# Kernel optimization log

Measured on AMD Instinct MI355X. Metric: run time of the kernel, lower is better.

The kernel has to match this reference:

```python
import jax, jax.numpy as jnp
import numpy as np
import math

D = 1024
H = 16
DH = D // H
B = 4
NSEQ = 1024
NSEG = 2
EXP = 4


def layer_norm(x, w, b=None, eps=1e-5):
    mu = jnp.mean(x, axis=-1, keepdims=True)
    var = jnp.mean((x - mu) ** 2, axis=-1, keepdims=True)
    y = (x - mu) * jax.lax.rsqrt(var + eps) * w
    return y + b if b is not None else y


def apply_rope(x, positions):
    # x: [B, L, H, Dh]; ESM-style rotate-half RoPE
    dh = x.shape[-1]
    inv_freq = 1.0 / (10000.0 ** (jnp.arange(0, dh, 2, dtype=jnp.float32) / dh))
    freqs = positions.astype(jnp.float32)[:, None] * inv_freq[None, :]  # [L, Dh/2]
    emb = jnp.concatenate([freqs, freqs], axis=-1)  # [L, Dh]
    cos = jnp.cos(emb)[None, :, None, :]
    sin = jnp.sin(emb)[None, :, None, :]
    x1, x2 = jnp.split(x, 2, axis=-1)
    return x * cos + jnp.concatenate([-x2, x1], axis=-1) * sin


def timestep_embedding(timesteps, embedding_dim=256, max_len=10000):
    # timesteps: [N]
    ts = timesteps * max_len
    half = embedding_dim // 2
    emb = math.log(max_len) / (half - 1)
    freqs = jnp.exp(jnp.arange(half, dtype=jnp.float32) * -emb)
    e = ts.astype(jnp.float32)[:, None] * freqs[None, :]
    return jnp.concatenate([jnp.sin(e), jnp.cos(e)], axis=1)  # [N, 256]


def make_autoregressive_attn_mask(batch_mask, n_seg):
    b, n_res = batch_mask.shape
    L = (n_seg + 1) * n_res
    causal = jnp.tril(jnp.ones((L, L), dtype=bool))[None, None]  # [1,1,L,L]
    tiled = jnp.tile(batch_mask, (1, n_seg + 1)).astype(bool)  # [B, L]
    key_valid = tiled[:, None, None, :]
    q_valid = tiled[:, None, :, None]
    allowed = causal & key_valid & q_valid  # [B,1,L,L]
    first_edit = (batch_mask[:, None, :] * batch_mask[:, :, None]).astype(bool)
    allowed = allowed.at[:, 0, :n_res, :n_res].set(first_edit)
    return allowed


def setup_inputs() -> dict:
    key = jax.random.key(0)
    ks = jax.random.split(key, 32)
    s = 0.02
    p = lambda i, shape: jax.random.normal(ks[i], shape, dtype=jnp.float32) * s
    inp = {
        'x_seq': jax.random.normal(ks[0], (B, NSEQ, D), dtype=jnp.float32),
        'x_struc': jax.random.normal(ks[1], (B, 1, D), dtype=jnp.float32),
        'temp': jax.random.uniform(ks[2], (B, 1, 1), dtype=jnp.float32),
        'mask': jnp.ones((B, NSEQ), dtype=jnp.float32),
        'ln_qs_w': jnp.ones((D,), jnp.float32), 'ln_qs_b': jnp.zeros((D,), jnp.float32),
        'W_qkv_seq': p(3, (D, 3 * D)),
        'ln_qt_w': jnp.ones((D,), jnp.float32), 'ln_qt_b': jnp.zeros((D,), jnp.float32),
        'W_qkv_struc': p(4, (D, 3 * D)),
        'q_ln_seq_w': jnp.ones((D,), jnp.float32), 'k_ln_seq_w': jnp.ones((D,), jnp.float32),
        'q_ln_struc_w': jnp.ones((D,), jnp.float32), 'k_ln_struc_w': jnp.ones((D,), jnp.float32),
        'W_out_seq': p(5, (D, D)), 'W_out_struc': p(6, (D, D)),
        'temp_w1': p(7, (1, D)), 'temp_b1': jnp.zeros((D,), jnp.float32),
        'temp_w2': p(8, (D, D)), 'temp_b2': jnp.zeros((D,), jnp.float32),
        'T_w1': p(9, (256, D)), 'T_b1': jnp.zeros((D,), jnp.float32),
        'T_w2': p(10, (D, D)), 'T_b2': jnp.zeros((D,), jnp.float32),
        'ffn_seq_ln_w': jnp.ones((D,), jnp.float32), 'ffn_seq_ln_b': jnp.zeros((D,), jnp.float32),
        'ffn_seq_w1': p(11, (D, EXP * D)), 'ffn_seq_w2': p(12, (EXP * D, D)),
        'ffn_struc_ln_w': jnp.ones((D,), jnp.float32), 'ffn_struc_ln_b': jnp.zeros((D,), jnp.float32),
        'ffn_struc_w1': p(13, (D, EXP * D)), 'ffn_struc_w2': p(14, (EXP * D, D)),
        'T': 1,
    }
    return inp


def reference(x_seq, x_struc, temp, mask,
              ln_qs_w, ln_qs_b, W_qkv_seq,
              ln_qt_w, ln_qt_b, W_qkv_struc,
              q_ln_seq_w, k_ln_seq_w, q_ln_struc_w, k_ln_struc_w,
              W_out_seq, W_out_struc,
              temp_w1, temp_b1, temp_w2, temp_b2,
              T_w1, T_b1, T_w2, T_b2,
              ffn_seq_ln_w, ffn_seq_ln_b, ffn_seq_w1, ffn_seq_w2,
              ffn_struc_ln_w, ffn_struc_ln_b, ffn_struc_w1, ffn_struc_w2,
              T):
    b, n_seq, d = x_seq.shape
    n_seg, index = NSEG, 0  # index=0 prefill path

    # --- seq track QKV (index == 0 only) ---
    qkv_seq = layer_norm(x_seq, ln_qs_w, ln_qs_b) @ W_qkv_seq
    q_s, k_s, v_s = jnp.split(qkv_seq, 3, axis=-1)
    q_s = layer_norm(q_s, q_ln_seq_w)
    k_s = layer_norm(k_s, k_ln_seq_w)
    pos_seq = jnp.arange(n_seq)
    q_s = apply_rope(q_s.reshape(b, n_seq, H, DH), pos_seq).reshape(b, n_seq, d)
    k_s = apply_rope(k_s.reshape(b, n_seq, H, DH), pos_seq).reshape(b, n_seq, d)

    # --- struc track conditioning + QKV ---
    position_T = jnp.arange(n_seg, dtype=jnp.float32) * T / 100.0
    T_input = jnp.repeat(position_T, n_seq)[index:index + 1]  # [1]
    x_norm = layer_norm(x_struc, ln_qt_w, ln_qt_b)
    temp_e = jax.nn.silu(temp @ temp_w1 + temp_b1) @ temp_w2 + temp_b2  # [B,1,D]
    t_emb = timestep_embedding(T_input)  # [1,256]
    T_e = jax.nn.silu(t_emb @ T_w1 + T_b1) @ T_w2 + T_b2  # [1,D]
    x_mod = x_norm + temp_e + T_e[None, :, :]
    qkv_t = x_mod @ W_qkv_struc
    q_t, k_t, v_t = jnp.split(qkv_t, 3, axis=-1)
    q_t = layer_norm(q_t, q_ln_struc_w)
    k_t = layer_norm(k_t, k_ln_struc_w)
    pos_res = jnp.tile(jnp.arange(n_seq), n_seg)[index:index + 1]  # [1]
    q_t = apply_rope(q_t.reshape(b, 1, H, DH), pos_res).reshape(b, 1, d)
    k_t = apply_rope(k_t.reshape(b, 1, H, DH), pos_res).reshape(b, 1, d)

    # --- KV cache contents for index 0: [seq tokens, struc token] ---
    keys = jnp.concatenate([k_s, k_t], axis=1)    # [B, N_seq+1, D]
    values = jnp.concatenate([v_s, v_t], axis=1)
    queries = jnp.concatenate([q_s, q_t], axis=1)

    to_heads = lambda t: t.reshape(b, -1, H, DH).transpose(0, 2, 1, 3)  # b h s d
    qh, kh, vh = to_heads(queries), to_heads(keys), to_heads(values)

    allowed = make_autoregressive_attn_mask(mask, n_seg)  # [B,1,L,L]
    Lq = n_seq + index + 1
    attn_mask = allowed[:, :, :Lq, :Lq]

    scale = 1.0 / math.sqrt(DH)
    scores = jnp.einsum('bhqd,bhkd->bhqk', qh, kh) * scale
    scores = jnp.where(attn_mask, scores, -1e9)
    probs = jax.nn.softmax(scores, axis=-1)
    ctx = jnp.einsum('bhqk,bhkd->bhqd', probs, vh)
    ctx = ctx.transpose(0, 2, 1, 3).reshape(b, Lq, d)

    out_seq = ctx[:, :n_seq] @ W_out_seq
    out_struc = ctx[:, n_seq:] @ W_out_struc

    # residuals (scaling_factor = 1)
    x_seq = x_seq + out_seq
    x_struc = x_struc + out_struc

    # GELU FFNs (LN -> Linear -> GELU -> Linear, no bias)
    h_seq = jax.nn.gelu(layer_norm(x_seq, ffn_seq_ln_w, ffn_seq_ln_b) @ ffn_seq_w1, approximate=False) @ ffn_seq_w2
    x_seq = x_seq + h_seq
    h_struc = jax.nn.gelu(layer_norm(x_struc, ffn_struc_ln_w, ffn_struc_ln_b) @ ffn_struc_w1, approximate=False) @ ffn_struc_w2
    x_struc = x_struc + h_struc

    return (x_seq, x_struc)
```

## Files before the change

kernel.cpp:

```cpp
#include <hip/hip_runtime.h>

typedef __attribute__((ext_vector_type(8))) short short8;
typedef __attribute__((ext_vector_type(4))) float f32x4;
typedef __attribute__((ext_vector_type(4))) unsigned short us4;

#define DEV static __device__ __forceinline__

DEV float bf2f(unsigned short u){ union{unsigned u; float f;} v; v.u=((unsigned)u)<<16; return v.f; }
DEV unsigned short f2bf(float f){ union{float f; unsigned u;} v; v.f=f; unsigned r=v.u+0x7fffu+((v.u>>16)&1u); return (unsigned short)(r>>16); }
DEV unsigned short f2bf_t(float f){ union{float f; unsigned u;} v; v.f=f; return (unsigned short)(v.u>>16); }
DEV float gelu_f(float x){ return 0.5f*x*(1.0f+erff(x*0.7071067811865475f)); }
DEV float silu_f(float x){ return x/(1.0f+__expf(-x)); }

DEV void gload16(const void* g, void* l){
  __builtin_amdgcn_global_load_lds((const __attribute__((address_space(1))) void*)g,
                                   (__attribute__((address_space(3))) void*)l, 16, 0, 0);
}

DEV void blk_reduce2(float &a, float &b){
  #pragma unroll
  for (int off=32; off>0; off>>=1){ a += __shfl_down(a,off); b += __shfl_down(b,off); }
  __shared__ float sa[4], sb[4];
  int w=threadIdx.x>>6;
  if((threadIdx.x&63)==0){ sa[w]=a; sb[w]=b; }
  __syncthreads();
  a=sa[0]+sa[1]+sa[2]+sa[3]; b=sb[0]+sb[1]+sb[2]+sb[3];
}

template<int OUTF32>
__global__ __launch_bounds__(256) void ln_rows(const float* __restrict__ x,
    const float* __restrict__ w, const float* __restrict__ bias, void* __restrict__ outp)
{
  int row=blockIdx.x, t=threadIdx.x;
  const float* xr = x + (size_t)row*1024;
  float4 v = *(const float4*)(xr + t*4);
  float s=v.x+v.y+v.z+v.w;
  float s2=v.x*v.x+v.y*v.y+v.z*v.z+v.w*v.w;
  blk_reduce2(s,s2);
  float mu=s*(1.0f/1024.0f);
  float rs=rsqrtf(s2*(1.0f/1024.0f)-mu*mu+1e-5f);
  int d0=t*4;
  const float* vp=(const float*)&v;
  float y[4];
  #pragma unroll
  for(int j=0;j<4;j++){ float bb = bias? bias[d0+j] : 0.0f; y[j]=(vp[j]-mu)*rs*w[d0+j]+bb; }
  if (OUTF32){
    float4 o; o.x=y[0];o.y=y[1];o.z=y[2];o.w=y[3];
    *(float4*)((float*)outp + (size_t)row*1024 + d0) = o;
  } else {
    us4 o;
    #pragma unroll
    for(int j=0;j<4;j++) o[j]=f2bf(y[j]);
    *(us4*)((unsigned short*)outp + (size_t)row*1024 + d0) = o;
  }
}

__global__ __launch_bounds__(256) void wtrans(const float* __restrict__ Bm,
    unsigned short* __restrict__ Bt, int K, int N)
{
  __shared__ float tile[32][33];
  int nb = blockIdx.x*32, kb = blockIdx.y*32;
  int tx = threadIdx.x&31, ty = threadIdx.x>>5;
  #pragma unroll
  for(int i=0;i<32;i+=8) tile[ty+i][tx] = Bm[(size_t)(kb+ty+i)*N + nb+tx];
  __syncthreads();
  #pragma unroll
  for(int i=0;i<32;i+=8) Bt[(size_t)(nb+ty+i)*K + kb+tx] = f2bf(tile[tx][ty+i]);
}

__global__ __launch_bounds__(256) void vtrans(const unsigned short* __restrict__ qkv,
    unsigned short* __restrict__ vT)
{
  __shared__ unsigned short tile[32][33];
  int d0 = blockIdx.x*32, tk0 = blockIdx.y*32, b = blockIdx.z;
  int tx = threadIdx.x&31, ty = threadIdx.x>>5;
  #pragma unroll
  for(int i=0;i<32;i+=8) tile[ty+i][tx] = qkv[(size_t)(b*1024+tk0+ty+i)*3072 + 2048 + d0+tx];
  __syncthreads();
  #pragma unroll
  for(int i=0;i<32;i+=8) vT[(size_t)(b*1024+d0+ty+i)*1024 + tk0+tx] = tile[tx][ty+i];
}

__global__ void rope_table(float* __restrict__ tab){
  int idx = blockIdx.x*256 + threadIdx.x;
  if (idx >= 1024*32) return;
  int pos = idx>>5, i = idx&31;
  float inv = exp2f(-(float)i * (13.287712379549449f/32.0f));
  float a = (float)pos*inv;
  tab[idx*2]   = cosf(a);
  tab[idx*2+1] = sinf(a);
}

__global__ __launch_bounds__(256) void qk_ln_rope(
    const unsigned short* __restrict__ qkv, const float* __restrict__ qw, const float* __restrict__ kw,
    const float* __restrict__ tab, unsigned short* __restrict__ qr, unsigned short* __restrict__ kr)
{
  __shared__ float lnr[1024];
  int row=blockIdx.x, part=blockIdx.y, t=threadIdx.x;
  const unsigned short* src = qkv + (size_t)row*3072 + part*1024 + t*4;
  us4 u = *(const us4*)src;
  float x[4];
  #pragma unroll
  for(int j=0;j<4;j++) x[j]=bf2f(u[j]);
  float s=x[0]+x[1]+x[2]+x[3];
  float s2=x[0]*x[0]+x[1]*x[1]+x[2]*x[2]+x[3]*x[3];
  blk_reduce2(s,s2);
  float mu=s*(1.0f/1024.0f);
  float rsg=rsqrtf(s2*(1.0f/1024.0f)-mu*mu+1e-5f);
  const float* w = part? kw : qw;
  int d0=t*4;
  #pragma unroll
  for(int j=0;j<4;j++) lnr[d0+j]=(x[j]-mu)*rsg*w[d0+j];
  __syncthreads();
  int n = row & 1023;
  unsigned short* dst = (part? kr: qr) + (size_t)row*1024 + d0;
  us4 o;
  #pragma unroll
  for(int j=0;j<4;j++){
    int d=d0+j, dh=d&63, fi=dh&31;
    float c=tab[(n*32+fi)*2], sn=tab[(n*32+fi)*2+1];
    float p=lnr[d^32];
    o[j]=f2bf(lnr[d]*c + ((dh<32)? -p : p)*sn);
  }
  *(us4*)dst = o;
}

template<int EPI>
__global__ __launch_bounds__(512) void gemm256(
    const unsigned short* __restrict__ A, int lda,
    const unsigned short* __restrict__ Bt, int ldb,
    int N, int K, void* Cout)
{
  __shared__ unsigned short As[16384];
  __shared__ unsigned short Bs[16384];
  const int t=threadIdx.x;
  int GX=gridDim.x, GY=gridDim.y, nwg=GX*GY;
  int bx, by;
  if (!(nwg&7)){
    int d = blockIdx.y*GX + blockIdx.x;
    int g = (d&7)*(nwg>>3) + (d>>3);
    bx = g%GX; by = g/GX;
  } else { bx = blockIdx.x; by = blockIdx.y; }
  const int m0=by*256, n0=bx*256;
  const int l=t&63, w=t>>6, lg=l>>4, lr=l&15;
  const int wr=w>>2, wc=w&3;
  const int srow=t>>3, sseg=(t&7)^((t>>3)&7);
  const f32x4 z4 = {0.f,0.f,0.f,0.f};
  f32x4 acc[8][4];
  #pragma unroll
  for(int i=0;i<8;i++)
    #pragma unroll
    for(int j=0;j<4;j++) acc[i][j]=z4;
  for (int k0=0;k0<K;k0+=64){
    __syncthreads();
    #pragma unroll
    for(int i=0;i<4;i++){
      gload16(A  + (size_t)(m0+srow+i*64)*lda + k0 + sseg*8, As + i*4096 + w*512);
      gload16(Bt + (size_t)(n0+srow+i*64)*ldb + k0 + sseg*8, Bs + i*4096 + w*512);
    }
    __syncthreads();
    #pragma unroll
    for(int ks=0;ks<2;ks++){
      short8 a[8], bfr[4];
      #pragma unroll
      for(int m=0;m<8;m++){
        int row=wr*128+m*16+lr;
        a[m] = *(const short8*)&As[row*64 + ((ks*4+lg)^(row&7))*8];
      }
      #pragma unroll
      for(int n=0;n<4;n++){
        int row=wc*64+n*16+lr;
        bfr[n] = *(const short8*)&Bs[row*64 + ((ks*4+lg)^(row&7))*8];
      }
      #pragma unroll
      for(int m=0;m<8;m++)
        #pragma unroll
        for(int n=0;n<4;n++)
          acc[m][n] = __builtin_amdgcn_mfma_f32_16x16x32_bf16(a[m], bfr[n], acc[m][n], 0,0,0);
    }
  }
  #pragma unroll
  for(int m=0;m<8;m++){
    #pragma unroll
    for(int n=0;n<4;n++){
      #pragma unroll
      for(int r=0;r<4;r++){
        int row=m0+wr*128+m*16+lg*4+r, col=n0+wc*64+n*16+lr;
        size_t idx=(size_t)row*N+col;
        float v=acc[m][n][r];
        if (EPI==2){ ((unsigned short*)Cout)[idx] = f2bf(gelu_f(v)); }
        else { ((unsigned short*)Cout)[idx] = f2bf(v); }
      }
    }
  }
}

template<int EPI>
__global__ __launch_bounds__(256) void gemm_bt(
    const unsigned short* __restrict__ A, int lda,
    const unsigned short* __restrict__ Bt, int ldb,
    int N, int K, void* Cout, const float* resp, void* Cout2)
{
  __shared__ unsigned short As[8192];
  __shared__ unsigned short Bs[8192];
  const int t=threadIdx.x;
  int GX=gridDim.x, GY=gridDim.y, nwg=GX*GY;
  int m0, n0;
  if (!((GX&7) || (nwg&63))){
    int d = blockIdx.y*GX + blockIdx.x;
    int xcd = d&7, j = d>>3;
    int g = xcd*(nwg>>3) + j;
    int chunk = g>>6, local = g&63;
    int chunks_x = GX>>3;
    int cx = chunk%chunks_x, cy = chunk/chunks_x;
    n0 = (cx*8 + (local&7))*128;
    m0 = (cy*8 + (local>>3))*128;
  } else {
    m0 = blockIdx.y*128; n0 = blockIdx.x*128;
  }
  const int kofs = blockIdx.z*K;
  unsigned short* Cb = (unsigned short*)(blockIdx.z ? Cout2 : Cout);
  const int l=t&63, w=t>>6, lg=l>>4, lr=l&15;
  const int wm=(w>>1)*64, wn=(w&1)*64;
  const int srow=t>>3, sseg=(t&7)^(srow&7);
  const f32x4 z4 = {0.f,0.f,0.f,0.f};
  f32x4 acc[4][4];
  #pragma unroll
  for(int i=0;i<4;i++)
    #pragma unroll
    for(int j=0;j<4;j++) acc[i][j]=z4;
  for (int k0=0;k0<K;k0+=64){
    __syncthreads();
    #pragma unroll
    for(int i=0;i<4;i++){
      gload16(A  + (size_t)(m0+srow+i*32)*lda + kofs + k0 + sseg*8, As + w*512 + i*2048);
      gload16(Bt + (size_t)(n0+srow+i*32)*ldb + kofs + k0 + sseg*8, Bs + w*512 + i*2048);
    }
    __syncthreads();
    #pragma unroll
    for(int ks=0;ks<2;ks++){
      short8 a[4], bfr[4];
      #pragma unroll
      for(int m=0;m<4;m++){
        int row=wm+m*16+lr;
        a[m] = *(const short8*)&As[row*64 + ((ks*4+lg)^(row&7))*8];
      }
      #pragma unroll
      for(int n=0;n<4;n++){
        int row=wn+n*16+lr;
        bfr[n] = *(const short8*)&Bs[row*64 + ((ks*4+lg)^(row&7))*8];
      }
      #pragma unroll
      for(int m=0;m<4;m++)
        #pragma unroll
        for(int n=0;n<4;n++)
          acc[m][n] = __builtin_amdgcn_mfma_f32_16x16x32_bf16(a[m], bfr[n], acc[m][n], 0,0,0);
    }
  }
  #pragma unroll
  for(int m=0;m<4;m++){
    #pragma unroll
    for(int n=0;n<4;n++){
      #pragma unroll
      for(int r=0;r<4;r++){
        int row=m0+wm+m*16+lg*4+r, col=n0+wn+n*16+lr;
        size_t idx=(size_t)row*N+col;
        float v=acc[m][n][r];
        if (EPI==1){ ((float*)Cout)[idx] = v + resp[idx]; }
        else if (EPI==2){ ((unsigned short*)Cout)[idx] = f2bf(gelu_f(v)); }
        else { Cb[idx] = f2bf(v); }
      }
    }
  }
}

__global__ __launch_bounds__(256) void comb2(float* __restrict__ out,
    const unsigned short* __restrict__ p0, const unsigned short* __restrict__ p1)
{
  size_t i = ((size_t)blockIdx.x*256 + threadIdx.x)*4;
  us4 a = *(const us4*)(p0+i);
  us4 b = *(const us4*)(p1+i);
  float4 o = *(float4*)(out+i);
  o.x += bf2f(a[0])+bf2f(b[0]);
  o.y += bf2f(a[1])+bf2f(b[1]);
  o.z += bf2f(a[2])+bf2f(b[2]);
  o.w += bf2f(a[3])+bf2f(b[3]);
  *(float4*)(out+i) = o;
}

__global__ __launch_bounds__(256) void flash_seq(
    const unsigned short* __restrict__ qr, const unsigned short* __restrict__ kr,
    const unsigned short* __restrict__ vT, unsigned short* __restrict__ ctx)
{
  __shared__ unsigned short Pl[4][32][64];
  const int t=threadIdx.x, w=t>>6, l=t&63, lg=l>>4, lr=l&15;
  int d = blockIdx.y*gridDim.x + blockIdx.x;
  int xcd = d&7;
  int g = xcd*64 + (d>>3);
  const int bh = g>>3, b = bh>>4, h = bh&15;
  const int q0 = (g&7)*128;
  const f32x4 z4 = {0.f,0.f,0.f,0.f};
  short8 qf[2][2];
  #pragma unroll
  for(int mf=0;mf<2;mf++)
    #pragma unroll
    for(int ks=0;ks<2;ks++)
      qf[mf][ks] = *(const short8*)(qr + (size_t)(b*1024 + q0 + w*32 + mf*16 + lr)*1024 + h*64 + ks*32 + lg*8);
  short8 ones;
  #pragma unroll
  for(int j=0;j<8;j++) ones[j] = (short)0x3F80;
  f32x4 o[2][4], lacc[2];
  #pragma unroll
  for(int mf=0;mf<2;mf++){
    lacc[mf]=z4;
    #pragma unroll
    for(int nd=0;nd<4;nd++) o[mf][nd]=z4;
  }
  for (int kv0=0;kv0<1024;kv0+=64){
    f32x4 s[2][4];
    #pragma unroll
    for(int mf=0;mf<2;mf++)
      #pragma unroll
      for(int nf=0;nf<4;nf++) s[mf][nf]=z4;
    #pragma unroll
    for(int ks=0;ks<2;ks++){
      #pragma unroll
      for(int nf=0;nf<4;nf++){
        short8 kf = *(const short8*)(kr + (size_t)(b*1024+kv0+nf*16+lr)*1024 + h*64 + ks*32 + lg*8);
        s[0][nf] = __builtin_amdgcn_mfma_f32_16x16x32_bf16(qf[0][ks], kf, s[0][nf],0,0,0);
        s[1][nf] = __builtin_amdgcn_mfma_f32_16x16x32_bf16(qf[1][ks], kf, s[1][nf],0,0,0);
      }
    }
    #pragma unroll
    for(int mf=0;mf<2;mf++)
      #pragma unroll
      for(int nf=0;nf<4;nf++)
        #pragma unroll
        for(int r=0;r<4;r++)
          s[mf][nf][r] = exp2f(fmaf(s[mf][nf][r], 0.18033688011112043f, -11.541560327111707f));
    #pragma unroll
    for(int mf=0;mf<2;mf++)
      #pragma unroll
      for(int nf=0;nf<4;nf++)
        #pragma unroll
        for(int r=0;r<4;r++){
          int prow = mf*16+lg*4+r;
          int col = (((nf*2+(lr>>3)) ^ (prow&7))<<3) + (lr&7);
          Pl[w][prow][col] = f2bf_t(s[mf][nf][r]);
        }
    #pragma unroll
    for(int ks2=0;ks2<2;ks2++){
      short8 pa0 = *(const short8*)&Pl[w][lr]   [((ks2*4+lg)^(lr&7))<<3];
      short8 pa1 = *(const short8*)&Pl[w][16+lr][((ks2*4+lg)^(lr&7))<<3];
      lacc[0] = __builtin_amdgcn_mfma_f32_16x16x32_bf16(pa0, ones, lacc[0],0,0,0);
      lacc[1] = __builtin_amdgcn_mfma_f32_16x16x32_bf16(pa1, ones, lacc[1],0,0,0);
      #pragma unroll
      for(int nd=0;nd<4;nd++){
        short8 vf = *(const short8*)(vT + (size_t)(b*1024 + h*64 + nd*16+lr)*1024 + kv0 + ks2*32 + lg*8);
        o[0][nd] = __builtin_amdgcn_mfma_f32_16x16x32_bf16(pa0, vf, o[0][nd],0,0,0);
        o[1][nd] = __builtin_amdgcn_mfma_f32_16x16x32_bf16(pa1, vf, o[1][nd],0,0,0);
      }
    }
  }
  #pragma unroll
  for(int mf=0;mf<2;mf++){
    #pragma unroll
    for(int r=0;r<4;r++){
      float inv = 1.0f/lacc[mf][r];
      #pragma unroll
      for(int nd=0;nd<4;nd++){
        ctx[(size_t)(b*1024 + q0 + w*32 + mf*16 + lg*4 + r)*1024 + h*64 + nd*16 + lr]
          = f2bf(o[mf][nd][r]*inv);
      }
    }
  }
}

__global__ __launch_bounds__(256) void struc_prep(const float* __restrict__ temp,
    const float* __restrict__ temp_w1, const float* __restrict__ temp_b1,
    const float* __restrict__ T_w1, const float* __restrict__ T_b1,
    float* __restrict__ sT, float* __restrict__ stemp)
{
  int j = blockIdx.x*256+threadIdx.x;
  float u=0.f;
  #pragma unroll 8
  for(int i=0;i<128;i++) u += T_w1[(size_t)(128+i)*1024 + j];
  sT[j] = silu_f(u + T_b1[j]);
  #pragma unroll
  for(int b=0;b<4;b++){ float z = temp[b]*temp_w1[j]+temp_b1[j]; stemp[b*1024+j]=silu_f(z); }
}

__global__ __launch_bounds__(256) void struc_te(
    const float* __restrict__ sT, const float* __restrict__ T_w2,
    const float* __restrict__ stemp, const float* __restrict__ temp_w2,
    float* __restrict__ tacc, float* __restrict__ eacc)
{
  __shared__ float As[4][64];
  const int t=threadIdx.x, n=blockIdx.x*256+t, k0=blockIdx.y*64;
  if (blockIdx.z==0){
    if (t<64) As[0][t]=sT[k0+t];
    __syncthreads();
    float acc=0.f;
    #pragma unroll 8
    for(int kk=0;kk<64;kk++) acc += As[0][kk]*T_w2[(size_t)(k0+kk)*1024 + n];
    atomicAdd(&tacc[n], acc);
  } else {
    { int m=t>>6, kk=t&63; As[m][kk]=stemp[m*1024 + k0+kk]; }
    __syncthreads();
    float acc[4]={0.f,0.f,0.f,0.f};
    #pragma unroll 8
    for(int kk=0;kk<64;kk++){
      float wv = temp_w2[(size_t)(k0+kk)*1024 + n];
      #pragma unroll
      for(int m=0;m<4;m++) acc[m] += As[m][kk]*wv;
    }
    #pragma unroll
    for(int m=0;m<4;m++) atomicAdd(&eacc[m*1024+n], acc[m]);
  }
}

__global__ __launch_bounds__(256) void struc_xmod(const float* __restrict__ xs,
    const float* __restrict__ qtw, const float* __restrict__ qtb,
    const float* __restrict__ eacc, const float* __restrict__ tacc,
    const float* __restrict__ temp_b2, const float* __restrict__ T_b2, float* __restrict__ xmod)
{
  int b=blockIdx.x, t=threadIdx.x;
  float4 v = *(const float4*)(xs + (size_t)b*1024 + t*4);
  float s=v.x+v.y+v.z+v.w, s2=v.x*v.x+v.y*v.y+v.z*v.z+v.w*v.w;
  blk_reduce2(s,s2);
  float mu=s*(1.0f/1024.0f);
  float rs=rsqrtf(s2*(1.0f/1024.0f)-mu*mu+1e-5f);
  const float* vp=(const float*)&v;
  #pragma unroll
  for(int j=0;j<4;j++){
    int d=t*4+j;
    xmod[b*1024+d] = (vp[j]-mu)*rs*qtw[d] + qtb[d] + eacc[b*1024+d] + tacc[d] + T_b2[d] + temp_b2[d];
  }
}

template<int MR, int GELU_A>
__global__ __launch_bounds__(256) void smallm_part(
    const float* __restrict__ A, const float* __restrict__ Bm,
    float* __restrict__ accp, int K, int N)
{
  __shared__ float As[MR][64];
  const int t=threadIdx.x;
  const int n = blockIdx.x*256 + t;
  const int k0 = blockIdx.y*64;
  if (t < MR*64){
    int m=t>>6, kk=t&63;
    float a = A[(size_t)m*K + k0+kk];
    As[m][kk] = GELU_A ? gelu_f(a) : a;
  }
  __syncthreads();
  float acc[MR];
  #pragma unroll
  for(int m=0;m<MR;m++) acc[m]=0.f;
  #pragma unroll 8
  for(int kk=0;kk<64;kk++){
    float wv = Bm[(size_t)(k0+kk)*N + n];
    #pragma unroll
    for(int m=0;m<MR;m++) acc[m] += As[m][kk]*wv;
  }
  #pragma unroll
  for(int m=0;m<MR;m++) atomicAdd(&accp[(size_t)m*N + n], acc[m]);
}

__global__ __launch_bounds__(256) void struc_qk_ln(float* qkv_t,
    const float* __restrict__ qw, const float* __restrict__ kw)
{
  int b=blockIdx.x>>1, part=blockIdx.x&1, t=threadIdx.x;
  float* xr = qkv_t + (size_t)b*3072 + part*1024;
  float4 v = *(const float4*)(xr + t*4);
  float s=v.x+v.y+v.z+v.w, s2=v.x*v.x+v.y*v.y+v.z*v.z+v.w*v.w;
  blk_reduce2(s,s2);
  float mu=s*(1.0f/1024.0f);
  float rsg=rsqrtf(s2*(1.0f/1024.0f)-mu*mu+1e-5f);
  const float* w = part? kw : qw;
  const float* vp=(const float*)&v;
  #pragma unroll
  for(int j=0;j<4;j++) xr[t*4+j]=(vp[j]-mu)*rsg*w[t*4+j];
}

__global__ __launch_bounds__(256) void struc_attn_part(
    const float* __restrict__ qkv_t, const unsigned short* __restrict__ kr,
    const unsigned short* __restrict__ vT, float* __restrict__ part)
{
  __shared__ float qs[64];
  __shared__ float pb[4][64];
  const int bh=blockIdx.x, b=bh>>4, h=bh&15;
  const int t=threadIdx.x, w=t>>6, l=t&63;
  if (t<64) qs[t]=qkv_t[(size_t)b*3072 + h*64 + t];
  __syncthreads();
  const int key = blockIdx.y*256 + w*64 + l;
  const unsigned short* krow = kr + (size_t)(b*1024+key)*1024 + h*64;
  float s=0.f;
  #pragma unroll
  for(int j=0;j<8;j++){
    short8 kk = *(const short8*)(krow + j*8);
    #pragma unroll
    for(int e=0;e<8;e++) s += qs[j*8+e]*bf2f((unsigned short)kk[e]);
  }
  s *= 0.125f;
  float mx=s;
  #pragma unroll
  for(int off=32;off>0;off>>=1) mx=fmaxf(mx,__shfl_xor(mx,off));
  float p=__expf(s-mx);
  float ls=p;
  #pragma unroll
  for(int off=32;off>0;off>>=1) ls+=__shfl_xor(ls,off);
  pb[w][l]=p;
  const int k0 = blockIdx.y*256 + w*64;
  float cacc=0.f;
  #pragma unroll
  for(int j=0;j<8;j++){
    short8 vv = *(const short8*)(vT + (size_t)(b*1024 + h*64 + l)*1024 + k0 + j*8);
    #pragma unroll
    for(int e=0;e<8;e++) cacc += pb[w][j*8+e]*bf2f((unsigned short)vv[e]);
  }
  float* pp = part + ((size_t)bh*16 + blockIdx.y*4 + w)*66;
  if(l==0){ pp[0]=mx; pp[1]=ls; }
  pp[2+l]=cacc;
}

__global__ __launch_bounds__(64) void struc_attn_comb(
    const float* __restrict__ part, const float* __restrict__ qkv_t, float* __restrict__ ctx_t)
{
  const int bh=blockIdx.x, b=bh>>4, h=bh&15, l=threadIdx.x;
  float M=-1e30f;
  #pragma unroll
  for(int i=0;i<16;i++) M=fmaxf(M, part[((size_t)bh*16+i)*66]);
  float lsum=0.f, cacc=0.f;
  #pragma unroll
  for(int i=0;i<16;i++){
    const float* pp = part + ((size_t)bh*16+i)*66;
    float f=__expf(pp[0]-M);
    lsum += pp[1]*f;
    cacc += pp[2+l]*f;
  }
  float qd=qkv_t[(size_t)b*3072 + h*64 + l];
  float kd=qkv_t[(size_t)b*3072 + 1024 + h*64 + l];
  float prod=qd*kd;
  #pragma unroll
  for(int off=32;off>0;off>>=1) prod+=__shfl_xor(prod,off);
  float st=prod*0.125f;
  float M2=fmaxf(M,st), fA=__expf(M-M2), pt=__expf(st-M2);
  cacc = cacc*fA + pt*qkv_t[(size_t)b*3072 + 2048 + h*64 + l];
  lsum = lsum*fA + pt;
  ctx_t[(size_t)b*1024 + h*64 + l] = cacc/lsum;
}

extern "C" void kernel_launch(void* const* d_in, const int* in_sizes, int n_in,
                              void* d_out, int out_size, void* d_ws, size_t ws_size,
                              hipStream_t stream){
  const float* x_seq    = (const float*)d_in[0];
  const float* x_struc  = (const float*)d_in[1];
  const float* temp     = (const float*)d_in[2];
  const float* ln_qs_w  = (const float*)d_in[4];
  const float* ln_qs_b  = (const float*)d_in[5];
  const float* W_qkv_seq= (const float*)d_in[6];
  const float* ln_qt_w  = (const float*)d_in[7];
  const float* ln_qt_b  = (const float*)d_in[8];
  const float* W_qkv_st = (const float*)d_in[9];
  const float* q_ln_seq_w=(const float*)d_in[10];
  const float* k_ln_seq_w=(const float*)d_in[11];
  const float* q_ln_st_w= (const float*)d_in[12];
  const float* k_ln_st_w= (const float*)d_in[13];
  const float* W_out_seq= (const float*)d_in[14];
  const float* W_out_st = (const float*)d_in[15];
  const float* temp_w1  = (const float*)d_in[16];
  const float* temp_b1  = (const float*)d_in[17];
  const float* temp_w2  = (const float*)d_in[18];
  const float* temp_b2  = (const float*)d_in[19];
  const float* T_w1     = (const float*)d_in[20];
  const float* T_b1     = (const float*)d_in[21];
  const float* T_w2     = (const float*)d_in[22];
  const float* T_b2     = (const float*)d_in[23];
  const float* ffn_s_ln_w=(const float*)d_in[24];
  const float* ffn_s_ln_b=(const float*)d_in[25];
  const float* ffn_s_w1 = (const float*)d_in[26];
  const float* ffn_s_w2 = (const float*)d_in[27];
  const float* ffn_t_ln_w=(const float*)d_in[28];
  const float* ffn_t_ln_b=(const float*)d_in[29];
  const float* ffn_t_w1 = (const float*)d_in[30];
  const float* ffn_t_w2 = (const float*)d_in[31];

  char* ws = (char*)d_ws;
  unsigned short* xn   = (unsigned short*)(ws + 0);
  unsigned short* qkv  = (unsigned short*)(ws + 8388608);
  unsigned short* qr   = (unsigned short*)(ws + 33554432);
  unsigned short* kr   = (unsigned short*)(ws + 41943040);
  unsigned short* ctx  = (unsigned short*)(ws + 50331648);
  float* tab   = (float*)(ws + 58720256);
  char* sm = ws + 58982400;
  float* sT    = (float*)(sm + 0);
  float* stemp = (float*)(sm + 4096);
  float* tacc  = (float*)(sm + 20544);
  float* eacc  = (float*)(sm + 24640);
  float* xmod  = (float*)(sm + 41024);
  float* qkvt  = (float*)(sm + 57408);
  float* ctxt  = (float*)(sm + 106560);
  float* xsn   = (float*)(sm + 122944);
  float* hsacc = (float*)(sm + 204864);
  float* part  = (float*)(sm + 270400);
  unsigned short* wqkvT = (unsigned short*)(ws + 50331648);
  unsigned short* woutT = (unsigned short*)(ws + 33554432);
  unsigned short* ffn1T = (unsigned short*)(ws + 41943040);
  unsigned short* ffn2T = (unsigned short*)(ws + 50331648);
  unsigned short* vT    = xn;
  unsigned short* hbuf  = qkv;
  unsigned short* pbuf0 = xn;
  unsigned short* pbuf1 = kr;
  float* outf = (float*)d_out;
  float* out_tail = outf + 4194304;

  ln_rows<0><<<4096,256,0,stream>>>(x_seq, ln_qs_w, ln_qs_b, xn);
  wtrans<<<dim3(96,32),256,0,stream>>>(W_qkv_seq, wqkvT, 1024, 3072);
  rope_table<<<128,256,0,stream>>>(tab);
  gemm256<0><<<dim3(12,16),512,0,stream>>>(xn, 1024, wqkvT, 1024, 3072, 1024, qkv);
  vtrans<<<dim3(32,32,4),256,0,stream>>>(qkv, vT);
  qk_ln_rope<<<dim3(4096,2),256,0,stream>>>(qkv, q_ln_seq_w, k_ln_seq_w, tab, qr, kr);
  flash_seq<<<dim3(8,64),256,0,stream>>>(qr, kr, vT, ctx);
  hipMemsetAsync(tacc, 0, 20480, stream);
  hipMemsetAsync(qkvt, 0, 12288*4, stream);
  struc_prep<<<4,256,0,stream>>>(temp, temp_w1, temp_b1, T_w1, T_b1, sT, stemp);
  struc_te<<<dim3(4,16,2),256,0,stream>>>(sT, T_w2, stemp, temp_w2, tacc, eacc);
  struc_xmod<<<4,256,0,stream>>>(x_struc, ln_qt_w, ln_qt_b, eacc, tacc, temp_b2, T_b2, xmod);
  smallm_part<4,0><<<dim3(12,16),256,0,stream>>>(xmod, W_qkv_st, qkvt, 1024, 3072);
  struc_qk_ln<<<8,256,0,stream>>>(qkvt, q_ln_st_w, k_ln_st_w);
  struc_attn_part<<<dim3(64,4),256,0,stream>>>(qkvt, kr, vT, part);
  struc_attn_comb<<<64,64,0,stream>>>(part, qkvt, ctxt);
  wtrans<<<dim3(32,32),256,0,stream>>>(W_out_seq, woutT, 1024, 1024);
  gemm_bt<1><<<dim3(8,32),256,0,stream>>>(ctx, 1024, woutT, 1024, 1024, 1024, outf, x_seq, nullptr);
  hipMemcpyAsync(out_tail, x_struc, 4096*4, hipMemcpyDeviceToDevice, stream);
  smallm_part<4,0><<<dim3(4,16),256,0,stream>>>(ctxt, W_out_st, out_tail, 1024, 1024);
  ln_rows<0><<<4096,256,0,stream>>>(outf, ffn_s_ln_w, ffn_s_ln_b, xn);
  wtrans<<<dim3(128,32),256,0,stream>>>(ffn_s_w1, ffn1T, 1024, 4096);
  gemm256<2><<<dim3(16,16),512,0,stream>>>(xn, 1024, ffn1T, 1024, 4096, 1024, hbuf);
  wtrans<<<dim3(32,128),256,0,stream>>>(ffn_s_w2, ffn2T, 4096, 1024);
  gemm_bt<0><<<dim3(8,32,2),256,0,stream>>>(hbuf, 4096, ffn2T, 4096, 1024, 2048, pbuf0, nullptr, pbuf1);
  comb2<<<4096,256,0,stream>>>(outf, pbuf0, pbuf1);
  ln_rows<1><<<4,256,0,stream>>>(out_tail, ffn_t_ln_w, ffn_t_ln_b, xsn);
  hipMemsetAsync(hsacc, 0, 16384*4, stream);
  smallm_part<4,0><<<dim3(16,16),256,0,stream>>>(xsn, ffn_t_w1, hsacc, 1024, 4096);
  smallm_part<4,1><<<dim3(4,64),256,0,stream>>>(hsacc, ffn_t_w2, out_tail, 4096, 1024);
  (void)in_sizes; (void)n_in; (void)out_size; (void)ws_size;
}
```

Measured before the change: 433.1 us.

## Double-buffer LDS tiles in both GEMM kernels to overlap loads with MFMA

Both GEMM kernels now keep two LDS buffers for the A and B tiles. The first K-tile is loaded before the loop, and each iteration prefetches the next tile into the other buffer while MFMAs run on the current one. This removes one barrier per iteration and hides global-to-LDS latency behind compute. The cost is double the LDS per block: gemm256 grows to 128KB, which likely allows only one block per CU where two fit before.

New measurement: 398.7 us. -7.9%, faster.

```diff
diff --git a/kernel.cpp b/kernel.cpp
--- a/kernel.cpp
+++ b/kernel.cpp
@@ -131,8 +131,8 @@
     const unsigned short* __restrict__ Bt, int ldb,
     int N, int K, void* Cout)
 {
-  __shared__ unsigned short As[16384];
-  __shared__ unsigned short Bs[16384];
+  __shared__ unsigned short As[2][16384];
+  __shared__ unsigned short Bs[2][16384];
   const int t=threadIdx.x;
   int GX=gridDim.x, GY=gridDim.y, nwg=GX*GY;
   int bx, by;
@@ -151,26 +151,33 @@
   for(int i=0;i<8;i++)
     #pragma unroll
     for(int j=0;j<4;j++) acc[i][j]=z4;
+  #pragma unroll
+  for(int i=0;i<4;i++){
+    gload16(A  + (size_t)(m0+srow+i*64)*lda + sseg*8, &As[0][i*4096 + w*512]);
+    gload16(Bt + (size_t)(n0+srow+i*64)*ldb + sseg*8, &Bs[0][i*4096 + w*512]);
+  }
+  int cur=0;
   for (int k0=0;k0<K;k0+=64){
     __syncthreads();
-    #pragma unroll
-    for(int i=0;i<4;i++){
-      gload16(A  + (size_t)(m0+srow+i*64)*lda + k0 + sseg*8, As + i*4096 + w*512);
-      gload16(Bt + (size_t)(n0+srow+i*64)*ldb + k0 + sseg*8, Bs + i*4096 + w*512);
-    }
-    __syncthreads();
+    if (k0+64 < K){
+      #pragma unroll
+      for(int i=0;i<4;i++){
+        gload16(A  + (size_t)(m0+srow+i*64)*lda + k0+64 + sseg*8, &As[cur^1][i*4096 + w*512]);
+        gload16(Bt + (size_t)(n0+srow+i*64)*ldb + k0+64 + sseg*8, &Bs[cur^1][i*4096 + w*512]);
+      }
+    }
     #pragma unroll
     for(int ks=0;ks<2;ks++){
       short8 a[8], bfr[4];
       #pragma unroll
       for(int m=0;m<8;m++){
         int row=wr*128+m*16+lr;
-        a[m] = *(const short8*)&As[row*64 + ((ks*4+lg)^(row&7))*8];
+        a[m] = *(const short8*)&As[cur][row*64 + ((ks*4+lg)^(row&7))*8];
       }
       #pragma unroll
       for(int n=0;n<4;n++){
         int row=wc*64+n*16+lr;
-        bfr[n] = *(const short8*)&Bs[row*64 + ((ks*4+lg)^(row&7))*8];
+        bfr[n] = *(const short8*)&Bs[cur][row*64 + ((ks*4+lg)^(row&7))*8];
       }
       #pragma unroll
       for(int m=0;m<8;m++)
@@ -178,6 +185,7 @@
         for(int n=0;n<4;n++)
           acc[m][n] = __builtin_amdgcn_mfma_f32_16x16x32_bf16(a[m], bfr[n], acc[m][n], 0,0,0);
     }
+    cur ^= 1;
   }
   #pragma unroll
   for(int m=0;m<8;m++){
@@ -201,8 +209,8 @@
     const unsigned short* __restrict__ Bt, int ldb,
     int N, int K, void* Cout, const float* resp, void* Cout2)
 {
-  __shared__ unsigned short As[8192];
-  __shared__ unsigned short Bs[8192];
+  __shared__ unsigned short As[2][8192];
+  __shared__ unsigned short Bs[2][8192];
   const int t=threadIdx.x;
   int GX=gridDim.x, GY=gridDim.y, nwg=GX*GY;
   int m0, n0;
@@ -229,26 +237,33 @@
   for(int i=0;i<4;i++)
     #pragma unroll
     for(int j=0;j<4;j++) acc[i][j]=z4;
+  #pragma unroll
+  for(int i=0;i<4;i++){
+    gload16(A  + (size_t)(m0+srow+i*32)*lda + kofs + sseg*8, &As[0][w*512 + i*2048]);
+    gload16(Bt + (size_t)(n0+srow+i*32)*ldb + kofs + sseg*8, &Bs[0][w*512 + i*2048]);
+  }
+  int cur=0;
   for (int k0=0;k0<K;k0+=64){
     __syncthreads();
-    #pragma unroll
-    for(int i=0;i<4;i++){
-      gload16(A  + (size_t)(m0+srow+i*32)*lda + kofs + k0 + sseg*8, As + w*512 + i*2048);
-      gload16(Bt + (size_t)(n0+srow+i*32)*ldb + kofs + k0 + sseg*8, Bs + w*512 + i*2048);
-    }
-    __syncthreads();
+    if (k0+64 < K){
+      #pragma unroll
+      for(int i=0;i<4;i++){
+        gload16(A  + (size_t)(m0+srow+i*32)*lda + kofs + k0+64 + sseg*8, &As[cur^1][w*512 + i*2048]);
+        gload16(Bt + (size_t)(n0+srow+i*32)*ldb + kofs + k0+64 + sseg*8, &Bs[cur^1][w*512 + i*2048]);
+      }
+    }
     #pragma unroll
     for(int ks=0;ks<2;ks++){
       short8 a[4], bfr[4];
       #pragma unroll
       for(int m=0;m<4;m++){
         int row=wm+m*16+lr;
-        a[m] = *(const short8*)&As[row*64 + ((ks*4+lg)^(row&7))*8];
+        a[m] = *(const short8*)&As[cur][row*64 + ((ks*4+lg)^(row&7))*8];
       }
       #pragma unroll
       for(int n=0;n<4;n++){
         int row=wn+n*16+lr;
-        bfr[n] = *(const short8*)&Bs[row*64 + ((ks*4+lg)^(row&7))*8];
+        bfr[n] = *(const short8*)&Bs[cur][row*64 + ((ks*4+lg)^(row&7))*8];
       }
       #pragma unroll
       for(int m=0;m<4;m++)
@@ -256,6 +271,7 @@
         for(int n=0;n<4;n++)
           acc[m][n] = __builtin_amdgcn_mfma_f32_16x16x32_bf16(a[m], bfr[n], acc[m][n], 0,0,0);
     }
+    cur ^= 1;
   }
   #pragma unroll
   for(int m=0;m<4;m++){
```
